# Kernel optimization log

Hardware: AMD Instinct MI355X
Metric: run time of the kernel (lower is better)

Reference implementation:

```python
import jax, jax.numpy as jnp
import numpy as np

D_IN = 1024
D_OUT = 1024

def setup_inputs() -> dict:
    key = jax.random.key(0)
    kx, kq, kk, kv = jax.random.split(key, 4)
    X = jax.random.normal(kx, (4, 2048, D_IN), dtype=jnp.float32)
    s = 1.0 / np.sqrt(D_IN)
    Wq = jax.random.uniform(kq, (D_IN, D_OUT), jnp.float32, -s, s)
    Wk = jax.random.uniform(kk, (D_IN, D_OUT), jnp.float32, -s, s)
    Wv = jax.random.uniform(kv, (D_IN, D_OUT), jnp.float32, -s, s)
    return {"X": X, "Wq": Wq, "Wk": Wk, "Wv": Wv}

def reference(X, Wq, Wk, Wv):
    # X: [b, s, d_in]; W*: [d_in, d_out] (torch Linear weight transposed)
    B, S, _ = X.shape
    q = jnp.einsum('bsd,de->bse', X, Wq)
    k = jnp.einsum('bsd,de->bse', X, Wk)
    v = jnp.einsum('bsd,de->bse', X, Wv)
    scores = jnp.einsum('bqe,bke->bqk', q, k)  # [b, s, s]
    causal = jnp.triu(jnp.ones((S, S), dtype=bool), k=1)
    scores = jnp.where(causal, -jnp.inf, scores)
    weights = jax.nn.softmax(scores / jnp.sqrt(jnp.asarray(k.shape[-1], scores.dtype)), axis=-1)
    # dropout p=0.0 (eval) -> identity
    return jnp.einsum('bqk,bke->bqe', weights, v)
```

## Files before the change

### kernel.cpp

```cpp
#include <hip/hip_runtime.h>
#include <cstdint>
#include <cmath>

typedef unsigned short u16;
typedef u16   u16x4  __attribute__((ext_vector_type(4)));
typedef u16   u16x8  __attribute__((ext_vector_type(8)));
typedef __bf16 bf16x8 __attribute__((ext_vector_type(8)));
typedef float f32x4  __attribute__((ext_vector_type(4)));

__device__ __forceinline__ u16 f2bf(float f) {
    uint32_t u = __builtin_bit_cast(uint32_t, f);
    u += 0x7fffu + ((u >> 16) & 1u);
    return (u16)(u >> 16);
}
__device__ __forceinline__ float bf2f(u16 v) {
    uint32_t u = ((uint32_t)v) << 16;
    return __builtin_bit_cast(float, u);
}
__device__ __forceinline__ void gload_lds16(const u16* g, u16* l) {
    __builtin_amdgcn_global_load_lds((const __attribute__((address_space(1))) void*)g,
                                     (__attribute__((address_space(3))) void*)l,
                                     16, 0, 0);
}

__global__ __launch_bounds__(256) void prep_kernel(const float* __restrict__ X,
                                                   const float* __restrict__ Wq,
                                                   const float* __restrict__ Wk,
                                                   const float* __restrict__ Wv,
                                                   u16* __restrict__ Xb,
                                                   u16* __restrict__ Wt) {
    __shared__ u16 tile[64 * 72];
    typedef float f4 __attribute__((ext_vector_type(4)));
    const int bid = blockIdx.x;
    if (bid < 8192) {
        const int idx = bid * 256 + threadIdx.x;
        f4 f = ((const f4*)X)[idx];
        u16x4 o;
        o[0] = f2bf(f[0]); o[1] = f2bf(f[1]); o[2] = f2bf(f[2]); o[3] = f2bf(f[3]);
        ((u16x4*)Xb)[idx] = o;
        return;
    }
    const int id = bid - 8192;
    const int z = id >> 8, rem = id & 255;
    const float* W = (z == 0) ? Wq : (z == 1) ? Wk : Wv;
    u16* out = Wt + ((size_t)z << 20);
    const int nt = (rem & 15) * 64, kt = (rem >> 4) * 64;
    const int t = threadIdx.x, r = t >> 2, cq = (t & 3) * 16;
    const float* src = W + (size_t)(kt + r) * 1024 + nt + cq;
#pragma unroll
    for (int q = 0; q < 4; q++) {
        f4 f = ((const f4*)src)[q];
        tile[r * 72 + cq + q * 4 + 0] = f2bf(f[0]);
        tile[r * 72 + cq + q * 4 + 1] = f2bf(f[1]);
        tile[r * 72 + cq + q * 4 + 2] = f2bf(f[2]);
        tile[r * 72 + cq + q * 4 + 3] = f2bf(f[3]);
    }
    __syncthreads();
    u16x8 o0, o1;
#pragma unroll
    for (int e = 0; e < 8; e++) { o0[e] = tile[(cq + e) * 72 + r]; o1[e] = tile[(cq + 8 + e) * 72 + r]; }
    u16* dst = out + (size_t)(nt + r) * 1024 + kt + cq;
    *(u16x8*)dst = o0;
    *(u16x8*)(dst + 8) = o1;
}

__global__ __launch_bounds__(512, 2) void qkv_gemm_kernel(const u16* __restrict__ Xb,
                                                          const u16* __restrict__ Wt,
                                                          u16* __restrict__ QKV) {
    __shared__ u16 lds[65536];
    const int bid = blockIdx.x;
    const int xcd = bid & 7, slot = bid >> 3;
    const int m0 = (xcd * 8 + (slot >> 3)) << 7;
    const int n0 = (slot & 7) << 7;

    const int tid = (int)threadIdx.x;
    const int w = tid >> 6, l = tid & 63;
    const int wm = w >> 2, wn = w & 3;

    const int srow = w * 16 + (l >> 3);
    const int scol = ((l & 7) ^ ((l >> 3) & 7)) * 8;
    const u16* gA  = Xb + (size_t)(m0 + srow) * 1024 + scol;
    const u16* gB0 = Wt + (size_t)(n0 + srow) * 1024 + scol;
    const u16* gB1 = gB0 + ((size_t)1 << 20);
    const u16* gB2 = gB0 + ((size_t)2 << 20);
    u16* const sA = lds + w * 1024;
    u16* const sB = lds + 16384 + w * 1024;

    const int c0 = ((l >> 4) ^ (l & 7)) * 8;
    const u16* const pa_ = lds + (wm * 64 + (l & 15)) * 64;
    const u16* const pb_ = lds + 16384 + (wn * 32 + (l & 15)) * 64;

    f32x4 acc[3][4][2] = {};
    bf16x8 a[4][2], b[2][2];

#define MFMA_ __builtin_amdgcn_mfma_f32_16x16x32_bf16
#define STG_A(P, T) \
    gload_lds16(gA + (size_t)(T) * 64,                    sA + (P) * 8192); \
    gload_lds16(gA + (size_t)(T) * 64 + (size_t)8 * 1024, sA + (P) * 8192 + 512);
#define STG_B(P, Z, GB, T) \
    gload_lds16(GB + (size_t)(T) * 64,                    sB + (Z) * 16384 + (P) * 8192); \
    gload_lds16(GB + (size_t)(T) * 64 + (size_t)8 * 1024, sB + (Z) * 16384 + (P) * 8192 + 512);
#define LD_A(P) \
    _Pragma("unroll") for (int m_ = 0; m_ < 4; m_++) { \
        a[m_][0] = *(const bf16x8*)(pa_ + (P) * 8192 + m_ * 1024 + c0); \
        a[m_][1] = *(const bf16x8*)(pa_ + (P) * 8192 + m_ * 1024 + (c0 ^ 32)); \
    }
#define LD_B(P, Z) \
    _Pragma("unroll") for (int n_ = 0; n_ < 2; n_++) { \
        b[n_][0] = *(const bf16x8*)(pb_ + (Z) * 16384 + (P) * 8192 + n_ * 1024 + c0); \
        b[n_][1] = *(const bf16x8*)(pb_ + (Z) * 16384 + (P) * 8192 + n_ * 1024 + (c0 ^ 32)); \
    }
#define MM(Z) \
    _Pragma("unroll") for (int m_ = 0; m_ < 4; m_++) { \
        _Pragma("unroll") for (int n_ = 0; n_ < 2; n_++) { \
            acc[Z][m_][n_] = MFMA_(a[m_][0], b[n_][0], acc[Z][m_][n_], 0, 0, 0); \
            acc[Z][m_][n_] = MFMA_(a[m_][1], b[n_][1], acc[Z][m_][n_], 0, 0, 0); \
        } \
    }
#define VM6 asm volatile("s_waitcnt vmcnt(6)" ::: "memory");
#define VM0 asm volatile("s_waitcnt vmcnt(0)" ::: "memory");
#define VMN
#define BAR __builtin_amdgcn_s_barrier();
#define PRIO1 __builtin_amdgcn_s_setprio(1);
#define PRIO0 __builtin_amdgcn_s_setprio(0);
#define TILE(P, S1, T1, S2, T2, VM3) \
    LD_A(P) LD_B(P, 0) \
    if (S1) { STG_B((P) ^ 1, 2, gB2, T1) } \
    BAR PRIO1 MM(0) PRIO0 BAR \
    LD_B(P, 1) \
    if (S2) { STG_A(P, T2) STG_B(P, 0, gB0, T2) } \
    BAR PRIO1 MM(1) PRIO0 BAR \
    LD_B(P, 2) \
    if (S2) { STG_B(P, 1, gB1, T2) } \
    VM3 \
    BAR PRIO1 MM(2) PRIO0 BAR

    STG_A(0, 0) STG_B(0, 0, gB0, 0) STG_B(0, 1, gB1, 0) STG_B(0, 2, gB2, 0)
    STG_A(1, 1) STG_B(1, 0, gB0, 1) STG_B(1, 1, gB1, 1)
    asm volatile("s_waitcnt vmcnt(6)" ::: "memory");
    __builtin_amdgcn_s_barrier();

#pragma unroll 1
    for (int i = 0; i < 7; ++i) {
        TILE(0, 1, 2 * i + 1, 1, 2 * i + 2, VM6)
        TILE(1, 1, 2 * i + 2, 1, 2 * i + 3, VM6)
    }
    TILE(0, 1, 15, 0, 0, VM0)
    TILE(1, 0, 0, 0, 0, VMN)

    const int row0 = m0 + wm * 64 + ((l >> 4) << 2);
    const int col0 = n0 + wn * 32 + (l & 15);
#pragma unroll
    for (int z = 0; z < 3; z++) {
        u16* C = QKV + ((size_t)z << 23);
#pragma unroll
        for (int m = 0; m < 4; m++)
#pragma unroll
            for (int r = 0; r < 4; r++) {
                u16* po = C + (size_t)(row0 + m * 16 + r) * 1024 + col0;
#pragma unroll
                for (int n = 0; n < 2; n++) po[n * 16] = f2bf(acc[z][m][n][r]);
            }
    }
#undef MFMA_
#undef STG_A
#undef STG_B
#undef LD_A
#undef LD_B
#undef MM
#undef VM6
#undef VM0
#undef VMN
#undef BAR
#undef PRIO1
#undef PRIO0
#undef TILE
}

__global__ __launch_bounds__(512, 2) void qk_tr_kernel(const u16* __restrict__ QKV,
                                                       u16* __restrict__ S,
                                                       u16* __restrict__ Vt,
                                                       float* __restrict__ rowsum) {
    __shared__ u16 lds[32768];
    const int bid = blockIdx.x;
    const int tid = (int)threadIdx.x;
    if (bid >= 544) {
        const int tile_id = (bid - 544) * 2 + (tid >> 8);
        const int t = tid & 255;
        const int b = tile_id >> 9, rem = tile_id & 511;
        const u16* src = QKV + ((size_t)2 << 23) + ((size_t)b << 21);
        u16* dst = Vt + ((size_t)b << 21);
        const int st = (rem & 31) * 64, et = (rem >> 5) * 64;
        u16 (*tile)[72] = (u16(*)[72])(lds + (tid >> 8) * 4608);
        const int r = t >> 2, cq = (t & 3) * 16;
        const u16* p = src + (size_t)(st + r) * 1024 + et + cq;
        u16x8 u0 = *(const u16x8*)p;
        u16x8 u1 = *(const u16x8*)(p + 8);
#pragma unroll
        for (int e = 0; e < 8; e++) { tile[r][cq + e] = u0[e]; tile[r][cq + 8 + e] = u1[e]; }
        __syncthreads();
        u16x8 o0, o1;
#pragma unroll
        for (int e = 0; e < 8; e++) { o0[e] = tile[cq + e][r]; o1[e] = tile[cq + 8 + e][r]; }
        u16* q = dst + (size_t)(et + r) * 2048 + st + cq;
        *(u16x8*)q = o0;
        *(u16x8*)(q + 8) = o1;
        return;
    }
    const int b = bid & 3;
    int t = bid >> 2;
    int it = 0;
    { int acc_ = 0; while (acc_ + it + 1 <= t) { acc_ += it + 1; it++; } t -= acc_; }
    const int jt = t;
    const int m0 = it * 128, n0 = jt * 128;
    const u16* Q = QKV + ((size_t)b << 21);
    const u16* K = QKV + ((size_t)1 << 23) + ((size_t)b << 21);
    u16* Sb = S + ((size_t)b << 22);
    float* rs = rowsum + (b << 11);

    const int w = tid >> 6, l = tid & 63;
    const int wm = w >> 2, wn = w & 3;
    const int srow = w * 16 + (l >> 3);
    const int scol = ((l & 7) ^ ((l >> 3) & 7)) * 8;
    const u16* gA = Q + (size_t)(m0 + srow) * 1024 + scol;
    const u16* gB = K + (size_t)(n0 + srow) * 1024 + scol;
    u16* const sA = lds + w * 1024;
    u16* const sB = lds + 16384 + w * 1024;
    const int c0 = ((l >> 4) ^ (l & 7)) * 8;
    const u16* const pa_ = lds + (wm * 64 + (l & 15)) * 64;
    const u16* const pb_ = lds + 16384 + (wn * 32 + (l & 15)) * 64;

    f32x4 acc[4][2] = {};
#define QSTG(T, BUF) \
    gload_lds16(gA + (size_t)(T) * 64,                    sA + (BUF) * 8192); \
    gload_lds16(gA + (size_t)(T) * 64 + (size_t)8 * 1024, sA + (BUF) * 8192 + 512); \
    gload_lds16(gB + (size_t)(T) * 64,                    sB + (BUF) * 8192); \
    gload_lds16(gB + (size_t)(T) * 64 + (size_t)8 * 1024, sB + (BUF) * 8192 + 512);

    QSTG(0, 0)
#pragma unroll 1
    for (int kt = 0; kt < 16; ++kt) {
        if (kt < 15) {
            QSTG(kt + 1, (kt + 1) & 1)
            asm volatile("s_waitcnt vmcnt(4)" ::: "memory");
        } else {
            asm volatile("s_waitcnt vmcnt(0)" ::: "memory");
        }
        __builtin_amdgcn_s_barrier();
        const int rb = (kt & 1) * 8192;
        bf16x8 a[4][2], bb[2][2];
#pragma unroll
        for (int m = 0; m < 4; m++) {
            a[m][0] = *(const bf16x8*)(pa_ + rb + m * 1024 + c0);
            a[m][1] = *(const bf16x8*)(pa_ + rb + m * 1024 + (c0 ^ 32));
        }
#pragma unroll
        for (int n = 0; n < 2; n++) {
            bb[n][0] = *(const bf16x8*)(pb_ + rb + n * 1024 + c0);
            bb[n][1] = *(const bf16x8*)(pb_ + rb + n * 1024 + (c0 ^ 32));
        }
        __builtin_amdgcn_s_setprio(1);
#pragma unroll
        for (int m = 0; m < 4; m++)
#pragma unroll
            for (int n = 0; n < 2; n++) {
                acc[m][n] = __builtin_amdgcn_mfma_f32_16x16x32_bf16(a[m][0], bb[n][0], acc[m][n], 0, 0, 0);
                acc[m][n] = __builtin_amdgcn_mfma_f32_16x16x32_bf16(a[m][1], bb[n][1], acc[m][n], 0, 0, 0);
            }
        __builtin_amdgcn_s_setprio(0);
        __builtin_amdgcn_s_barrier();
    }
#undef QSTG
    const float sc = 0.03125f * 1.44269504088896f;
    const bool diag = (it == jt);
    const int row0g = m0 + wm * 64 + ((l >> 4) << 2);
    const int col0g = n0 + wn * 32 + (l & 15);
#pragma unroll
    for (int m = 0; m < 4; m++)
#pragma unroll
        for (int r = 0; r < 4; r++) {
            const int row = row0g + m * 16 + r;
            u16* po = Sb + (size_t)row * 2048 + col0g;
            float psum = 0.f;
#pragma unroll
            for (int n = 0; n < 2; n++) {
                const int col = col0g + n * 16;
                const float p = (diag && col > row) ? 0.f : exp2f(acc[m][n][r] * sc);
                po[n * 16] = f2bf(p);
                psum += p;
            }
            psum += __shfl_xor(psum, 1, 64);
            psum += __shfl_xor(psum, 2, 64);
            psum += __shfl_xor(psum, 4, 64);
            psum += __shfl_xor(psum, 8, 64);
            if ((l & 15) == 0) atomicAdd(rs + row, psum);
        }
}

__device__ __forceinline__ void pv_tile128(const u16* __restrict__ Pb,
                                           const u16* __restrict__ Vb,
                                           float* __restrict__ Ob,
                                           const float* __restrict__ rs,
                                           u16* __restrict__ lds,
                                           const int it, const int n0) {
    const int tid = (int)threadIdx.x;
    const int w = tid >> 6, l = tid & 63;
    const int wm = w >> 2, wn = w & 3;
    const int nk = 2 * (it + 1);
    const int m0 = it * 128;

    const int srow = w * 16 + (l >> 3);
    const int scol = ((l & 7) ^ ((l >> 3) & 7)) * 8;
    const u16* gA = Pb + (size_t)(m0 + srow) * 2048 + scol;
    const u16* gB = Vb + (size_t)(n0 + srow) * 2048 + scol;
    u16* const sA = lds + w * 1024;
    u16* const sB = lds + 24576 + w * 1024;

    const int c0 = ((l >> 4) ^ (l & 7)) * 8;
    const u16* const pa_ = lds + (wm * 64 + (l & 15)) * 64;
    const u16* const pb_ = lds + 24576 + (wn * 32 + (l & 15)) * 64;

    f32x4 acc[4][2] = {};

#define PSTG(T, BUF) \
    gload_lds16(gA + (size_t)(T) * 64,                    sA + (BUF) * 8192); \
    gload_lds16(gA + (size_t)(T) * 64 + (size_t)8 * 2048, sA + (BUF) * 8192 + 512); \
    gload_lds16(gB + (size_t)(T) * 64,                    sB + (BUF) * 8192); \
    gload_lds16(gB + (size_t)(T) * 64 + (size_t)8 * 2048, sB + (BUF) * 8192 + 512);

    PSTG(0, 0) PSTG(1, 1)
    asm volatile("s_waitcnt vmcnt(4)" ::: "memory");
    __builtin_amdgcn_s_barrier();

    int bufR = 0, bufW = 2;
#pragma unroll 1
    for (int t = 0; t < nk; ++t) {
        bf16x8 a[4][2], b[2][2];
#pragma unroll
        for (int m = 0; m < 4; m++) {
            a[m][0] = *(const bf16x8*)(pa_ + bufR * 8192 + m * 1024 + c0);
            a[m][1] = *(const bf16x8*)(pa_ + bufR * 8192 + m * 1024 + (c0 ^ 32));
        }
#pragma unroll
        for (int n = 0; n < 2; n++) {
            b[n][0] = *(const bf16x8*)(pb_ + bufR * 8192 + n * 1024 + c0);
            b[n][1] = *(const bf16x8*)(pb_ + bufR * 8192 + n * 1024 + (c0 ^ 32));
        }
        if (t < nk - 2) {
            PSTG(t + 2, bufW)
            asm volatile("s_waitcnt vmcnt(4)" ::: "memory");
        } else {
            asm volatile("s_waitcnt vmcnt(0)" ::: "memory");
        }
        __builtin_amdgcn_s_barrier();
        __builtin_amdgcn_s_setprio(1);
#pragma unroll
        for (int m = 0; m < 4; m++)
#pragma unroll
            for (int n = 0; n < 2; n++) {
                acc[m][n] = __builtin_amdgcn_mfma_f32_16x16x32_bf16(a[m][0], b[n][0], acc[m][n], 0, 0, 0);
                acc[m][n] = __builtin_amdgcn_mfma_f32_16x16x32_bf16(a[m][1], b[n][1], acc[m][n], 0, 0, 0);
            }
        __builtin_amdgcn_s_setprio(0);
        __builtin_amdgcn_s_barrier();
        bufR = (bufR == 2) ? 0 : bufR + 1;
        bufW = (bufW == 2) ? 0 : bufW + 1;
    }
#undef PSTG

    const int row0 = m0 + wm * 64 + ((l >> 4) << 2);
    const int col0 = n0 + wn * 32 + (l & 15);
#pragma unroll
    for (int m = 0; m < 4; m++) {
        const f32x4 rsv = *(const f32x4*)(rs + row0 + m * 16);
#pragma unroll
        for (int r = 0; r < 4; r++) {
            const float inv = 1.f / rsv[r];
            float* po = Ob + (size_t)(row0 + m * 16 + r) * 1024 + col0;
#pragma unroll
            for (int n = 0; n < 2; n++) po[n * 16] = acc[m][n][r] * inv;
        }
    }
}

__global__ __launch_bounds__(512, 2) void pv_gemm_kernel(const u16* __restrict__ P,
                                                         const u16* __restrict__ Vt,
                                                         float* __restrict__ O,
                                                         const float* __restrict__ rowsum) {
    __shared__ u16 lds[49152];
    const int bid = blockIdx.x;
    const int xcd = bid & 7, slot = bid >> 3;
    const int combo = xcd * 4 + (slot >> 3);
    const int n0 = (slot & 7) * 128;
    const int pair = combo >> 2, b = combo & 3;
    const u16* Pb = P + ((size_t)b << 22);
    const u16* Vb = Vt + ((size_t)b << 21);
    float* Ob = O + ((size_t)b << 21);
    const float* rb = rowsum + (b << 11);
    pv_tile128(Pb, Vb, Ob, rb, lds, 15 - pair, n0);
    pv_tile128(Pb, Vb, Ob, rb, lds, pair, n0);
}

extern "C" void kernel_launch(void* const* d_in, const int* in_sizes, int n_in,
                              void* d_out, int out_size, void* d_ws, size_t ws_size,
                              hipStream_t stream) {
    const float* X  = (const float*)d_in[0];
    const float* Wq = (const float*)d_in[1];
    const float* Wk = (const float*)d_in[2];
    const float* Wv = (const float*)d_in[3];
    float* out = (float*)d_out;

    u16* ws  = (u16*)d_ws;
    u16* Xb  = ws;
    u16* Wt  = Xb + ((size_t)1 << 23);
    u16* QKV = Wt + 3 * ((size_t)1 << 20);
    u16* S   = QKV + 3 * ((size_t)1 << 23);
    u16* Vt  = Xb;
    float* rowsum = (float*)(S + ((size_t)1 << 24));

    hipMemsetAsync(rowsum, 0, 4 * 2048 * sizeof(float), stream);
    prep_kernel<<<8960, 256, 0, stream>>>(X, Wq, Wk, Wv, Xb, Wt);
    qkv_gemm_kernel<<<512, 512, 0, stream>>>(Xb, Wt, QKV);
    qk_tr_kernel<<<1568, 512, 0, stream>>>(QKV, S, Vt, rowsum);
    pv_gemm_kernel<<<256, 512, 0, stream>>>(S, Vt, out, rowsum);
}
```

Baseline: 220.8 us.

## Fold rowsum memset into prep kernel, coarsen X conversion, pair causal tiles

Drops the separate hipMemsetAsync by having one extra prep block zero the rowsum buffer, which removes one launch from the sequence. The X fp32-to-bf16 conversion now does four vectors per thread, cutting its block count by a factor of four. The QK tile index mapping is changed so each group of eight consecutive blocks pairs a long row band (it=15-x) with a short one (it=x), replacing the serial triangular-decode loop and aiming to balance causal work across CUs. The mapping is only correct for a 16-tile triangle.

```diff
diff --git a/kernel.cpp b/kernel.cpp
--- a/kernel.cpp
+++ b/kernel.cpp
@@ -28,19 +28,31 @@
                                                    const float* __restrict__ Wk,
                                                    const float* __restrict__ Wv,
                                                    u16* __restrict__ Xb,
-                                                   u16* __restrict__ Wt) {
+                                                   u16* __restrict__ Wt,
+                                                   float* __restrict__ rowsum) {
     __shared__ u16 tile[64 * 72];
     typedef float f4 __attribute__((ext_vector_type(4)));
     const int bid = blockIdx.x;
-    if (bid < 8192) {
-        const int idx = bid * 256 + threadIdx.x;
-        f4 f = ((const f4*)X)[idx];
-        u16x4 o;
-        o[0] = f2bf(f[0]); o[1] = f2bf(f[1]); o[2] = f2bf(f[2]); o[3] = f2bf(f[3]);
-        ((u16x4*)Xb)[idx] = o;
+    if (bid < 2048) {
+        const int base = bid * 1024 + threadIdx.x;
+#pragma unroll
+        for (int k = 0; k < 4; k++) {
+            const int idx = base + k * 256;
+            f4 f = ((const f4*)X)[idx];
+            u16x4 o;
+            o[0] = f2bf(f[0]); o[1] = f2bf(f[1]); o[2] = f2bf(f[2]); o[3] = f2bf(f[3]);
+            ((u16x4*)Xb)[idx] = o;
+        }
         return;
     }
-    const int id = bid - 8192;
+    if (bid == 2816) {
+        f32x4 z = {0.f, 0.f, 0.f, 0.f};
+        f32x4* p = (f32x4*)rowsum;
+#pragma unroll
+        for (int k = 0; k < 8; k++) p[k * 256 + threadIdx.x] = z;
+        return;
+    }
+    const int id = bid - 2048;
     const int z = id >> 8, rem = id & 255;
     const float* W = (z == 0) ? Wq : (z == 1) ? Wk : Wv;
     u16* out = Wt + ((size_t)z << 20);
@@ -207,11 +219,13 @@
         *(u16x8*)(q + 8) = o1;
         return;
     }
-    const int b = bid & 3;
-    int t = bid >> 2;
-    int it = 0;
-    { int acc_ = 0; while (acc_ + it + 1 <= t) { acc_ += it + 1; it++; } t -= acc_; }
-    const int jt = t;
+    const int x = bid & 7;
+    const int idx = bid >> 3;
+    const int b = idx & 3;
+    const int u = idx >> 2;
+    int it, jt;
+    if (u < 16 - x) { it = 15 - x; jt = u; }
+    else            { it = x;      jt = u - (16 - x); }
     const int m0 = it * 128, n0 = jt * 128;
     const u16* Q = QKV + ((size_t)b << 21);
     const u16* K = QKV + ((size_t)1 << 23) + ((size_t)b << 21);
@@ -418,8 +432,7 @@
     u16* Vt  = Xb;
     float* rowsum = (float*)(S + ((size_t)1 << 24));
 
-    hipMemsetAsync(rowsum, 0, 4 * 2048 * sizeof(float), stream);
-    prep_kernel<<<8960, 256, 0, stream>>>(X, Wq, Wk, Wv, Xb, Wt);
+    prep_kernel<<<2817, 256, 0, stream>>>(X, Wq, Wk, Wv, Xb, Wt, rowsum);
     qkv_gemm_kernel<<<512, 512, 0, stream>>>(Xb, Wt, QKV);
     qk_tr_kernel<<<1568, 512, 0, stream>>>(QKV, S, Vt, rowsum);
     pv_gemm_kernel<<<256, 512, 0, stream>>>(S, Vt, out, rowsum);
```

New measurement: 218.8 us. About the same (-0.9%).
